# Kernel optimization log

Hardware: AMD Instinct MI355X
Metric: run time of the kernel (lower is better)

## Reference

```python
import jax, jax.numpy as jnp
import numpy as np

EMBED_DIM = 1024
NUM_HEADS = 16
HEAD_DIM = EMBED_DIM // NUM_HEADS
SCALE = HEAD_DIM ** -0.5


def setup_inputs() -> dict:
    key = jax.random.key(0)
    ks = jax.random.split(key, 7)
    B, S, D = 4, 2048, EMBED_DIM
    return {
        "x": jax.random.normal(ks[0], (B, S, D), dtype=jnp.float32),
        "gamma": jnp.ones((D,), dtype=jnp.float32),
        "beta": jnp.zeros((D,), dtype=jnp.float32),
        "w_qkv": jax.random.normal(ks[1], (D, 3 * D), dtype=jnp.float32) * (D ** -0.5),
        "b_qkv": jax.random.normal(ks[2], (3 * D,), dtype=jnp.float32) * 0.02,
        "w_proj": jax.random.normal(ks[3], (D, D), dtype=jnp.float32) * (D ** -0.5),
        "b_proj": jax.random.normal(ks[4], (D,), dtype=jnp.float32) * 0.02,
    }


def reference(x, gamma, beta, w_qkv, b_qkv, w_proj, b_proj):
    B, S, D = x.shape
    # pre-norm LayerNorm (eps=1e-5, torch default)
    mu = jnp.mean(x, axis=-1, keepdims=True)
    var = jnp.mean(jnp.square(x - mu), axis=-1, keepdims=True)
    xn = (x - mu) * jax.lax.rsqrt(var + 1e-5) * gamma + beta
    # fused QKV projection -> (3, B, H, S, hd)
    qkv = (xn @ w_qkv + b_qkv).reshape(B, S, 3, NUM_HEADS, HEAD_DIM)
    qkv = jnp.transpose(qkv, (2, 0, 3, 1, 4))
    q, k, v = qkv[0], qkv[1], qkv[2]
    scores = jnp.einsum("bhqd,bhkd->bhqk", q, k) * SCALE
    attn = jax.nn.softmax(scores, axis=-1)  # dropout p=0 -> no-op
    ctx = jnp.einsum("bhqk,bhkd->bhqd", attn, v)
    ctx = jnp.transpose(ctx, (0, 2, 1, 3)).reshape(B, S, D)
    return ctx @ w_proj + b_proj
```

## Files before the change

kernel.cpp:

```cpp
#include <hip/hip_runtime.h>

typedef unsigned short ushort_t;
typedef __attribute__((ext_vector_type(8))) short bf16x8;
typedef __attribute__((ext_vector_type(4))) float f32x4;
typedef __attribute__((ext_vector_type(16))) float f32x16;
typedef __attribute__((ext_vector_type(2))) __bf16 bf16v2;

#define BN 4
#define SEQ 2048
#define DIM 1024
#define NH 16
#define HDIM 64
#define MROWS (BN*SEQ)
#define QSCALE 0.18033688011112042f

__device__ __forceinline__ float bf2f(ushort_t s){ return __uint_as_float(((unsigned)s) << 16); }
__device__ __forceinline__ ushort_t f2bf(float f){
  unsigned u = __float_as_uint(f);
  u += 0x7fffu + ((u >> 16) & 1u);
  return (ushort_t)(u >> 16);
}
__device__ __forceinline__ unsigned pack2(float a, float b){
  return (unsigned)f2bf(a) | ((unsigned)f2bf(b) << 16);
}

#define GLL16(gp, lp) __builtin_amdgcn_global_load_lds( \
    (const __attribute__((address_space(1))) void*)(gp), \
    (__attribute__((address_space(3))) void*)(lp), 16, 0, 0)

__global__ __launch_bounds__(256) void ln_kernel(const float* __restrict__ x,
                                                 const float* __restrict__ gamma,
                                                 const float* __restrict__ beta,
                                                 ushort_t* __restrict__ xnb)
{
  int row = blockIdx.x;
  int t = threadIdx.x;
  float4 v = ((const float4*)(x + (size_t)row * DIM))[t];
  float s = v.x+v.y+v.z+v.w;
  float ss = v.x*v.x+v.y*v.y+v.z*v.z+v.w*v.w;
  #pragma unroll
  for (int o = 32; o > 0; o >>= 1){ s += __shfl_down(s, o); ss += __shfl_down(ss, o); }
  __shared__ float red[10];
  int wid = t >> 6;
  if ((t & 63) == 0){ red[wid] = s; red[4+wid] = ss; }
  __syncthreads();
  if (t == 0){
    float S0 = red[0]+red[1]+red[2]+red[3];
    float SS = red[4]+red[5]+red[6]+red[7];
    float mu = S0 * (1.f/DIM);
    float var = SS * (1.f/DIM) - mu*mu;
    red[8] = mu; red[9] = rsqrtf(var + 1e-5f);
  }
  __syncthreads();
  float mu = red[8], rstd = red[9];
  float4 g = ((const float4*)gamma)[t];
  float4 b = ((const float4*)beta)[t];
  float f0 = (v.x - mu)*rstd*g.x + b.x;
  float f1 = (v.y - mu)*rstd*g.y + b.y;
  float f2 = (v.z - mu)*rstd*g.z + b.z;
  float f3 = (v.w - mu)*rstd*g.w + b.w;
  *(uint2*)(xnb + (size_t)row*DIM + t*4) = make_uint2(pack2(f0,f1), pack2(f2,f3));
}

__global__ __launch_bounds__(256) void cvt_t(const float* __restrict__ src,
                                             ushort_t* __restrict__ dst,
                                             int K, int N, float qscale)
{
  __shared__ float tile[64][65];
  int k0 = blockIdx.y*64, n0 = blockIdx.x*64;
  float sc = (n0 < 1024) ? qscale : 1.f;
  int t = threadIdx.x;
  int c = (t & 15) * 4, r = t >> 4;
  #pragma unroll
  for (int p = 0; p < 4; p++){
    float4 v = *(const float4*)(src + (size_t)(k0 + r + p*16)*N + n0 + c);
    tile[r+p*16][c]   = v.x; tile[r+p*16][c+1] = v.y;
    tile[r+p*16][c+2] = v.z; tile[r+p*16][c+3] = v.w;
  }
  __syncthreads();
  #pragma unroll
  for (int p = 0; p < 4; p++){
    int nn = r + p*16;
    ushort4 o;
    o.x = f2bf(tile[c+0][nn]*sc); o.y = f2bf(tile[c+1][nn]*sc);
    o.z = f2bf(tile[c+2][nn]*sc); o.w = f2bf(tile[c+3][nn]*sc);
    *(ushort4*)(dst + (size_t)(n0+nn)*K + k0 + c) = o;
  }
}

template<int MODE, int NCOLS>
__global__ __launch_bounds__(256) void mfma_gemm(
    const ushort_t* __restrict__ A,
    const ushort_t* __restrict__ BT,
    const float* __restrict__ bias,
    void* __restrict__ Cv,
    ushort_t* __restrict__ Vv)
{
  __shared__ __align__(16) unsigned char smem[32768];
  ushort_t* AsL = (ushort_t*)smem;
  ushort_t* BsL = (ushort_t*)(smem + 16384);

  int t = threadIdx.x;
  int lane = t & 63, w = t >> 6;
  int col = lane & 15, quad = lane >> 4;
  int n0 = blockIdx.x * 128, m0 = blockIdx.y * 128;

  f32x4 acc[4][4];
  #pragma unroll
  for (int i = 0; i < 4; i++)
    #pragma unroll
    for (int j = 0; j < 4; j++) acc[i][j] = (f32x4){0.f,0.f,0.f,0.f};

  int mbase = (w & 1)*64 + col;
  int nbase = (w >> 1)*64 + col;

  int rloc = lane >> 3, g8 = lane & 7;
  int cA = ((g8 ^ rloc) << 3);
  const ushort_t* gA[4]; const ushort_t* gB[4];
  #pragma unroll
  for (int s = 0; s < 4; s++){
    int row = (4*w + s)*8 + rloc;
    gA[s] = A  + (size_t)(m0 + row)*DIM + cA;
    gB[s] = BT + (size_t)(n0 + row)*DIM + cA;
  }

  int pposA = ((quad      ^ (col & 7)) << 3);
  int pposB = (((4 + quad) ^ (col & 7)) << 3);

  for (int k0 = 0; k0 < DIM; k0 += 64){
    __syncthreads();
    #pragma unroll
    for (int s = 0; s < 4; s++){
      GLL16(gA[s] + k0, smem         + (4*w + s)*1024);
      GLL16(gB[s] + k0, smem + 16384 + (4*w + s)*1024);
    }
    __syncthreads();

    bf16x8 af[4], bfr[4];
    #pragma unroll
    for (int i = 0; i < 4; i++){
      af[i]  = *(const bf16x8*)&AsL[(mbase + i*16)*64 + pposA];
      bfr[i] = *(const bf16x8*)&BsL[(nbase + i*16)*64 + pposA];
    }
    #pragma unroll
    for (int mt = 0; mt < 4; mt++)
      #pragma unroll
      for (int nt = 0; nt < 4; nt++)
        acc[mt][nt] = __builtin_amdgcn_mfma_f32_16x16x32_bf16(af[mt], bfr[nt], acc[mt][nt], 0, 0, 0);
    #pragma unroll
    for (int i = 0; i < 4; i++){
      af[i]  = *(const bf16x8*)&AsL[(mbase + i*16)*64 + pposB];
      bfr[i] = *(const bf16x8*)&BsL[(nbase + i*16)*64 + pposB];
    }
    #pragma unroll
    for (int mt = 0; mt < 4; mt++)
      #pragma unroll
      for (int nt = 0; nt < 4; nt++)
        acc[mt][nt] = __builtin_amdgcn_mfma_f32_16x16x32_bf16(af[mt], bfr[nt], acc[mt][nt], 0, 0, 0);
  }

  float bscale = (MODE == 2 && n0 < 1024) ? QSCALE : 1.f;
  float bv[4];
  #pragma unroll
  for (int nt = 0; nt < 4; nt++) bv[nt] = bias[n0 + (w>>1)*64 + nt*16 + col] * bscale;

  if (MODE == 2){
    ushort_t (*Cs)[136] = (ushort_t(*)[136])smem;
    ushort_t* C = (ushort_t*)Cv;
    bool isV = (n0 >= 2*DIM);
    #pragma unroll
    for (int ph = 0; ph < 2; ph++){
      __syncthreads();
      if ((w & 1) == ph){
        #pragma unroll
        for (int mt = 0; mt < 4; mt++)
          #pragma unroll
          for (int nt = 0; nt < 4; nt++)
            #pragma unroll
            for (int r = 0; r < 4; r++)
              Cs[mt*16 + quad*4 + r][(w>>1)*64 + nt*16 + col] = f2bf(acc[mt][nt][r] + bv[nt]);
      }
      __syncthreads();
      if (isV){
        int mb = m0 + ph*64;
        int b_ = mb >> 11, sc = (mb & (SEQ-1)) >> 6;
        #pragma unroll
        for (int p = 0; p < 4; p++){
          int id2 = p*256 + t;
          int dloc = id2 >> 3;
          int sg = (id2 & 7) * 8;
          int n = n0 + dloc;
          int hh = (n >> 6) & 15, dd2 = n & 63;
          int bh2 = b_*NH + hh;
          uint4 uu;
          uu.x = (unsigned)Cs[sg+0][dloc] | ((unsigned)Cs[sg+1][dloc] << 16);
          uu.y = (unsigned)Cs[sg+2][dloc] | ((unsigned)Cs[sg+3][dloc] << 16);
          uu.z = (unsigned)Cs[sg+4][dloc] | ((unsigned)Cs[sg+5][dloc] << 16);
          uu.w = (unsigned)Cs[sg+6][dloc] | ((unsigned)Cs[sg+7][dloc] << 16);
          *(uint4*)&Vv[((size_t)(bh2*32 + sc))*HDIM*64 + dd2*64 + sg] = uu;
        }
      } else {
        #pragma unroll
        for (int p = 0; p < 4; p++){
          int id = p*256 + t;
          int row = id >> 4, cc = id & 15;
          uint4 u = *(const uint4*)&Cs[row][cc*8];
          int m = m0 + ph*64 + row;
          int n = n0 + cc*8;
          int which = n >> 10, hh = (n >> 6) & 15, d = n & 63;
          int b_ = m >> 11, s_ = m & (SEQ-1);
          *(uint4*)&C[((((size_t)which*BN + b_)*NH + hh)*SEQ + s_)*HDIM + d] = u;
        }
      }
    }
  } else {
    float (*Cf)[132] = (float(*)[132])smem;
    float* C = (float*)Cv;
    #pragma unroll
    for (int ph = 0; ph < 4; ph++){
      __syncthreads();
      if ((w & 1) == (ph >> 1)){
        #pragma unroll
        for (int mi = 0; mi < 2; mi++){
          int mt = (ph & 1)*2 + mi;
          #pragma unroll
          for (int nt = 0; nt < 4; nt++)
            #pragma unroll
            for (int r = 0; r < 4; r++)
              Cf[mi*16 + quad*4 + r][(w>>1)*64 + nt*16 + col] = acc[mt][nt][r] + bv[nt];
        }
      }
      __syncthreads();
      #pragma unroll
      for (int p = 0; p < 4; p++){
        int id = p*256 + t;
        int row = id >> 5, cc = id & 31;
        float4 v = *(const float4*)&Cf[row][cc*4];
        int m = m0 + ph*32 + row;
        *(float4*)(C + (size_t)m*NCOLS + n0 + cc*4) = v;
      }
    }
  }
}

__global__ __launch_bounds__(512) void attn_kernel(const ushort_t* __restrict__ qkv,
                                                   const ushort_t* __restrict__ vtp,
                                                   ushort_t* __restrict__ ctx)
{
  __shared__ __align__(16) unsigned char lds[32768];

  int t = threadIdx.x;
  int lane = t & 63, w = t >> 6;
  int m32 = lane & 31, half = lane >> 5;
  int r7 = m32 & 7;
  int d15 = m32 & 15;
  int id = blockIdx.x;
  int bh = (id & 7) | ((id >> 6) << 3);
  int qb = (id >> 3) & 7;

  const size_t PL = (size_t)BN * NH * SEQ * HDIM;
  const ushort_t* Qg = qkv + (size_t)bh * (SEQ * HDIM);
  const ushort_t* Kg = Qg + PL;
  const ushort_t* Vt = vtp + (size_t)bh * 32 * (HDIM * 64);
  int qbase = qb*256 + w*32;

  bf16x8 qf[4];
  #pragma unroll
  for (int c = 0; c < 4; c++)
    qf[c] = *(const bf16x8*)(Qg + (size_t)(qbase + m32)*HDIM + c*16 + half*8);

  bf16x8 ones;
  #pragma unroll
  for (int i = 0; i < 8; i++) ones[i] = (short)0x3F80;

  f32x16 accO[2], accL;
  #pragma unroll
  for (int i = 0; i < 2; i++)
    #pragma unroll
    for (int r = 0; r < 16; r++) accO[i][r] = 0.f;
  #pragma unroll
  for (int r = 0; r < 16; r++) accL[r] = 0.f;

  int srow = t >> 3, och = t & 7;
  const ushort_t* kp0 = Kg + (size_t)srow*HDIM + och*8;
  const ushort_t* vp0 = Vt + (size_t)srow*64 + och*8;
  int wofsK = srow*64 + ((och ^ (srow & 7)) << 3);
  int wofsV = srow*64 + ((och ^ ((srow >> 1) & 7)) << 3);
  bool vswap = (srow & 1);

  uint4 kr = *(const uint4*)kp0;
  uint4 vr = *(const uint4*)vp0;
  *(uint4*)&((ushort_t*)lds)[wofsK] = kr;
  {
    uint4 vs;
    vs.x = vswap ? vr.z : vr.x;  vs.y = vswap ? vr.w : vr.y;
    vs.z = vswap ? vr.x : vr.z;  vs.w = vswap ? vr.y : vr.w;
    *(uint4*)&((ushort_t*)(lds + 16384))[wofsV] = vs;
  }
  kr = *(const uint4*)(kp0 + (size_t)64*HDIM);
  vr = *(const uint4*)(vp0 + (size_t)HDIM*64);
  __syncthreads();

  for (int kt = 0; kt < 32; kt++){
    const ushort_t* Kc = (const ushort_t*)(lds + ((kt & 1) << 13));
    const ushort_t* Vc = (const ushort_t*)(lds + 16384 + ((kt & 1) << 13));

    if (kt < 31){
      ushort_t* Kn = (ushort_t*)(lds + (((kt + 1) & 1) << 13));
      ushort_t* Vn = (ushort_t*)(lds + 16384 + (((kt + 1) & 1) << 13));
      *(uint4*)&Kn[wofsK] = kr;
      uint4 vs;
      vs.x = vswap ? vr.z : vr.x;  vs.y = vswap ? vr.w : vr.y;
      vs.z = vswap ? vr.x : vr.z;  vs.w = vswap ? vr.y : vr.w;
      *(uint4*)&Vn[wofsV] = vs;
      int nk = (kt + 2 <= 31) ? kt + 2 : 31;
      kr = *(const uint4*)(kp0 + (size_t)nk*64*HDIM);
      vr = *(const uint4*)(vp0 + (size_t)nk*HDIM*64);
    }

    bf16x8 pb[4];
    #pragma unroll
    for (int mt = 0; mt < 2; mt++){
      f32x16 z;
      #pragma unroll
      for (int r = 0; r < 16; r++) z[r] = 0.f;
      int rowb = (mt*32 + m32) * 64;
      __builtin_amdgcn_s_setprio(1);
      #pragma unroll
      for (int c = 0; c < 4; c++){
        bf16x8 af = *(const bf16x8*)&Kc[rowb + (((2*c + half) ^ r7) << 3)];
        z = __builtin_amdgcn_mfma_f32_32x32x16_bf16(af, qf[c], z, 0, 0, 0);
      }
      __builtin_amdgcn_s_setprio(0);
      unsigned u[8];
      #pragma unroll
      for (int i = 0; i < 8; i++){
        float p0 = __builtin_amdgcn_exp2f(z[2*i]);
        float p1 = __builtin_amdgcn_exp2f(z[2*i+1]);
        bf16v2 hh; hh.x = (__bf16)p0; hh.y = (__bf16)p1;
        u[i] = __builtin_bit_cast(unsigned, hh);
      }
      #pragma unroll
      for (int cc = 0; cc < 2; cc++){
        union { uint4 q; bf16x8 b; } cvt;
        cvt.q = make_uint4(u[4*cc+0], u[4*cc+1], u[4*cc+2], u[4*cc+3]);
        pb[mt*2 + cc] = cvt.b;
      }
    }

    __builtin_amdgcn_s_setprio(1);
    #pragma unroll
    for (int kc = 0; kc < 4; kc++){
      accL = __builtin_amdgcn_mfma_f32_32x32x16_bf16(ones, pb[kc], accL, 0, 0, 0);
      #pragma unroll
      for (int md = 0; md < 2; md++){
        int rowb = (md*32 + m32) * 64;
        union { bf16x8 v8; uint2 u2[2]; } vv;
        vv.u2[0] = *(const uint2*)&Vc[rowb + (((4*kc     + half) ^ d15) << 2)];
        vv.u2[1] = *(const uint2*)&Vc[rowb + (((4*kc + 2 + half) ^ d15) << 2)];
        accO[md] = __builtin_amdgcn_mfma_f32_32x32x16_bf16(vv.v8, pb[kc], accO[md], 0, 0, 0);
      }
    }
    __builtin_amdgcn_s_setprio(0);

    if (kt < 31) __syncthreads();
  }

  __syncthreads();
  float inv = 1.f / accL[0];

  ushort_t* Osm = (ushort_t*)(lds + w*4096);
  #pragma unroll
  for (int md = 0; md < 2; md++)
    #pragma unroll
    for (int g = 0; g < 4; g++){
      int j16 = g + 4*md;
      int p = j16 ^ r7;
      unsigned lo = pack2(accO[md][4*g+0]*inv, accO[md][4*g+1]*inv);
      unsigned hi = pack2(accO[md][4*g+2]*inv, accO[md][4*g+3]*inv);
      *(uint2*)&Osm[m32*64 + p*8 + half*4] = make_uint2(lo, hi);
    }

  int b_ = bh >> 4, h_ = bh & 15;
  #pragma unroll
  for (int k = 0; k < 4; k++){
    int row = k*8 + (lane >> 3);
    int p = (lane & 7) ^ (row & 7);
    uint4 u = *(const uint4*)&Osm[row*64 + p*8];
    *(uint4*)(ctx + ((size_t)(b_*SEQ + qb*256 + w*32 + row))*DIM + h_*HDIM + (lane & 7)*8) = u;
  }
}

extern "C" void kernel_launch(void* const* d_in, const int* in_sizes, int n_in,
                              void* d_out, int out_size, void* d_ws, size_t ws_size,
                              hipStream_t stream)
{
  const float* x      = (const float*)d_in[0];
  const float* gamma  = (const float*)d_in[1];
  const float* beta   = (const float*)d_in[2];
  const float* w_qkv  = (const float*)d_in[3];
  const float* b_qkv  = (const float*)d_in[4];
  const float* w_proj = (const float*)d_in[5];
  const float* b_proj = (const float*)d_in[6];

  char* ws = (char*)d_ws;
  ushort_t* wqkvT  = (ushort_t*)ws;
  ushort_t* qkv    = (ushort_t*)(ws + 16u*1024*1024);
  ushort_t* vt     = (ushort_t*)(ws + 48u*1024*1024);
  ushort_t* ctx    = (ushort_t*)ws;
  ushort_t* wprojT = (ushort_t*)(ws + 16u*1024*1024);
  ushort_t* xnb    = (ushort_t*)d_out;

  ln_kernel<<<MROWS, 256, 0, stream>>>(x, gamma, beta, xnb);
  cvt_t<<<dim3(3*DIM/64, DIM/64), 256, 0, stream>>>(w_qkv, wqkvT, DIM, 3*DIM, QSCALE);
  mfma_gemm<2, 3*DIM><<<dim3(3*DIM/128, MROWS/128), 256, 0, stream>>>(
      xnb, wqkvT, b_qkv, qkv, vt);
  attn_kernel<<<BN*NH*(SEQ/256), 512, 0, stream>>>(qkv, vt, ctx);
  cvt_t<<<dim3(DIM/64, DIM/64), 256, 0, stream>>>(w_proj, wprojT, DIM, DIM, 1.f);
  mfma_gemm<0, DIM><<<dim3(DIM/128, MROWS/128), 256, 0, stream>>>(
      ctx, wprojT, b_proj, d_out, nullptr);
}
```

Baseline: 279.1 us.

## Fuse LayerNorm with QKV weight conversion and remap GEMM tiles per XCD

Merges the LayerNorm kernel and the QKV weight transpose/convert kernel into a single launch, with extra blocks that handle the weight tiles. This removes one launch and lets the two independent jobs overlap. Both GEMMs now use a 1D grid whose block index is remapped so that each of the 8 XCDs (taking the block id modulo 8) handles a fixed group of N-column tiles, which is meant to improve L2 reuse of the weight tiles. The cost is extra index arithmetic, and the fused kernel declares shared memory it only needs in its second branch.

Result: no change. 284.4 us (+1.9%).

```diff
diff --git a/kernel.cpp b/kernel.cpp
--- a/kernel.cpp
+++ b/kernel.cpp
@@ -28,38 +28,64 @@
     (const __attribute__((address_space(1))) void*)(gp), \
     (__attribute__((address_space(3))) void*)(lp), 16, 0, 0)
 
-__global__ __launch_bounds__(256) void ln_kernel(const float* __restrict__ x,
-                                                 const float* __restrict__ gamma,
-                                                 const float* __restrict__ beta,
-                                                 ushort_t* __restrict__ xnb)
+__global__ __launch_bounds__(256) void ln_cvt_kernel(const float* __restrict__ x,
+                                                     const float* __restrict__ gamma,
+                                                     const float* __restrict__ beta,
+                                                     ushort_t* __restrict__ xnb,
+                                                     const float* __restrict__ wq,
+                                                     ushort_t* __restrict__ wqkvT)
 {
-  int row = blockIdx.x;
+  int bid = blockIdx.x;
   int t = threadIdx.x;
-  float4 v = ((const float4*)(x + (size_t)row * DIM))[t];
-  float s = v.x+v.y+v.z+v.w;
-  float ss = v.x*v.x+v.y*v.y+v.z*v.z+v.w*v.w;
-  #pragma unroll
-  for (int o = 32; o > 0; o >>= 1){ s += __shfl_down(s, o); ss += __shfl_down(ss, o); }
-  __shared__ float red[10];
-  int wid = t >> 6;
-  if ((t & 63) == 0){ red[wid] = s; red[4+wid] = ss; }
-  __syncthreads();
-  if (t == 0){
-    float S0 = red[0]+red[1]+red[2]+red[3];
-    float SS = red[4]+red[5]+red[6]+red[7];
-    float mu = S0 * (1.f/DIM);
-    float var = SS * (1.f/DIM) - mu*mu;
-    red[8] = mu; red[9] = rsqrtf(var + 1e-5f);
-  }
-  __syncthreads();
-  float mu = red[8], rstd = red[9];
-  float4 g = ((const float4*)gamma)[t];
-  float4 b = ((const float4*)beta)[t];
-  float f0 = (v.x - mu)*rstd*g.x + b.x;
-  float f1 = (v.y - mu)*rstd*g.y + b.y;
-  float f2 = (v.z - mu)*rstd*g.z + b.z;
-  float f3 = (v.w - mu)*rstd*g.w + b.w;
-  *(uint2*)(xnb + (size_t)row*DIM + t*4) = make_uint2(pack2(f0,f1), pack2(f2,f3));
+  if (bid < MROWS){
+    int row = bid;
+    float4 v = ((const float4*)(x + (size_t)row * DIM))[t];
+    float s = v.x+v.y+v.z+v.w;
+    float ss = v.x*v.x+v.y*v.y+v.z*v.z+v.w*v.w;
+    #pragma unroll
+    for (int o = 32; o > 0; o >>= 1){ s += __shfl_down(s, o); ss += __shfl_down(ss, o); }
+    __shared__ float red[10];
+    int wid = t >> 6;
+    if ((t & 63) == 0){ red[wid] = s; red[4+wid] = ss; }
+    __syncthreads();
+    if (t == 0){
+      float S0 = red[0]+red[1]+red[2]+red[3];
+      float SS = red[4]+red[5]+red[6]+red[7];
+      float mu = S0 * (1.f/DIM);
+      float var = SS * (1.f/DIM) - mu*mu;
+      red[8] = mu; red[9] = rsqrtf(var + 1e-5f);
+    }
+    __syncthreads();
+    float mu = red[8], rstd = red[9];
+    float4 g = ((const float4*)gamma)[t];
+    float4 b = ((const float4*)beta)[t];
+    float f0 = (v.x - mu)*rstd*g.x + b.x;
+    float f1 = (v.y - mu)*rstd*g.y + b.y;
+    float f2 = (v.z - mu)*rstd*g.z + b.z;
+    float f3 = (v.w - mu)*rstd*g.w + b.w;
+    *(uint2*)(xnb + (size_t)row*DIM + t*4) = make_uint2(pack2(f0,f1), pack2(f2,f3));
+  } else {
+    __shared__ float tile[64][65];
+    int id = bid - MROWS;
+    int n0 = (id % 48) * 64, k0 = (id / 48) * 64;
+    float sc = (n0 < 1024) ? QSCALE : 1.f;
+    int c = (t & 15) * 4, r = t >> 4;
+    #pragma unroll
+    for (int p = 0; p < 4; p++){
+      float4 v = *(const float4*)(wq + (size_t)(k0 + r + p*16)*(3*DIM) + n0 + c);
+      tile[r+p*16][c]   = v.x; tile[r+p*16][c+1] = v.y;
+      tile[r+p*16][c+2] = v.z; tile[r+p*16][c+3] = v.w;
+    }
+    __syncthreads();
+    #pragma unroll
+    for (int p = 0; p < 4; p++){
+      int nn = r + p*16;
+      ushort4 o;
+      o.x = f2bf(tile[c+0][nn]*sc); o.y = f2bf(tile[c+1][nn]*sc);
+      o.z = f2bf(tile[c+2][nn]*sc); o.w = f2bf(tile[c+3][nn]*sc);
+      *(ushort4*)(wqkvT + (size_t)(n0+nn)*DIM + k0 + c) = o;
+    }
+  }
 }
 
 __global__ __launch_bounds__(256) void cvt_t(const float* __restrict__ src,
@@ -103,7 +129,13 @@
   int t = threadIdx.x;
   int lane = t & 63, w = t >> 6;
   int col = lane & 15, quad = lane >> 4;
-  int n0 = blockIdx.x * 128, m0 = blockIdx.y * 128;
+
+  int bid = blockIdx.x;
+  int xcd = bid & 7, idx = bid >> 3;
+  int nb, mb;
+  if (MODE == 2){ nb = xcd*3 + (idx % 3); mb = idx / 3; }
+  else          { nb = xcd;               mb = idx;     }
+  int n0 = nb * 128, m0 = mb * 128;
 
   f32x4 acc[4][4];
   #pragma unroll
@@ -182,8 +214,8 @@
       }
       __syncthreads();
       if (isV){
-        int mb = m0 + ph*64;
-        int b_ = mb >> 11, sc = (mb & (SEQ-1)) >> 6;
+        int mrow = m0 + ph*64;
+        int b_ = mrow >> 11, sc = (mrow & (SEQ-1)) >> 6;
         #pragma unroll
         for (int p = 0; p < 4; p++){
           int id2 = p*256 + t;
@@ -411,12 +443,9 @@
   ushort_t* wprojT = (ushort_t*)(ws + 16u*1024*1024);
   ushort_t* xnb    = (ushort_t*)d_out;
 
-  ln_kernel<<<MROWS, 256, 0, stream>>>(x, gamma, beta, xnb);
-  cvt_t<<<dim3(3*DIM/64, DIM/64), 256, 0, stream>>>(w_qkv, wqkvT, DIM, 3*DIM, QSCALE);
-  mfma_gemm<2, 3*DIM><<<dim3(3*DIM/128, MROWS/128), 256, 0, stream>>>(
-      xnb, wqkvT, b_qkv, qkv, vt);
+  ln_cvt_kernel<<<MROWS + 768, 256, 0, stream>>>(x, gamma, beta, xnb, w_qkv, wqkvT);
+  mfma_gemm<2, 3*DIM><<<1536, 256, 0, stream>>>(xnb, wqkvT, b_qkv, qkv, vt);
   attn_kernel<<<BN*NH*(SEQ/256), 512, 0, stream>>>(qkv, vt, ctx);
   cvt_t<<<dim3(DIM/64, DIM/64), 256, 0, stream>>>(w_proj, wprojT, DIM, DIM, 1.f);
-  mfma_gemm<0, DIM><<<dim3(DIM/128, MROWS/128), 256, 0, stream>>>(
-      ctx, wprojT, b_proj, d_out, nullptr);
-}
+  mfma_gemm<0, DIM><<<512, 256, 0, stream>>>(ctx, wprojT, b_proj, d_out, nullptr);
+}
```
